# Optimization experiments

Hardware: AMD Instinct MI355X
Metric: run time of the kernel (lower is better)

Reference implementation:

```python
import jax, jax.numpy as jnp
import numpy as np

N = 20000
E = 320000
NEG_SLOPE = 0.2
BN_EPS = 1e-5


def _segment_softmax(e, dst, n):
    # e: [E, H] attention logits, dst: [E] destination node ids
    m = jax.ops.segment_max(e, dst, num_segments=n)           # [N, H]
    ex = jnp.exp(e - m[dst])                                   # [E, H]
    s = jax.ops.segment_sum(ex, dst, num_segments=n)          # [N, H]
    return ex / s[dst]


def gat_conv(x, src, dst, W, a_src, a_dst, b, heads, out_ch):
    # PyG GATConv (concat=True): h = x @ W reshaped to [N, H, C]
    n = x.shape[0]
    h = (x @ W).reshape(n, heads, out_ch)                      # [N, H, C]
    al_s = jnp.einsum('nhc,hc->nh', h, a_src)                  # [N, H]
    al_d = jnp.einsum('nhc,hc->nh', h, a_dst)
    e = jax.nn.leaky_relu(al_s[src] + al_d[dst], NEG_SLOPE)    # [E, H]
    alpha = _segment_softmax(e, dst, n)                        # [E, H]
    msg = h[src] * alpha[:, :, None]                           # [E, H, C]
    out = jax.ops.segment_sum(msg, dst, num_segments=n)        # [N, H, C]
    return out.reshape(n, heads * out_ch) + b


def batch_norm(x, gamma, beta):
    mu = jnp.mean(x, axis=0)
    var = jnp.mean((x - mu) ** 2, axis=0)  # biased, as torch BN training
    return gamma * (x - mu) * jax.lax.rsqrt(var + BN_EPS) + beta


def setup_inputs() -> dict:
    key = jax.random.key(0)
    ks = jax.random.split(key, 16)
    F_in, H1, C1 = 128, 8, 64
    D = H1 * C1  # 512
    OUT = 2
    def gl(k, shape, fan):
        return jax.random.normal(k, shape, dtype=jnp.float32) / np.sqrt(fan)
    x = jax.random.normal(ks[0], (N, F_in), dtype=jnp.float32)
    edge_index = jax.random.randint(ks[1], (2, E), 0, N, dtype=jnp.int64)
    return {
        'x': x, 'edge_index': edge_index,
        'W1': gl(ks[2], (F_in, H1 * C1), F_in),
        'a1s': gl(ks[3], (H1, C1), C1), 'a1d': gl(ks[4], (H1, C1), C1),
        'b1': jnp.zeros((D,), jnp.float32),
        'W2': gl(ks[5], (D, D), D),
        'a2s': gl(ks[6], (1, D), D), 'a2d': gl(ks[7], (1, D), D),
        'b2': jnp.zeros((D,), jnp.float32),
        'fc1_w': gl(ks[8], (D, D), D), 'fc1_b': jnp.zeros((D,), jnp.float32),
        'g1': jnp.ones((D,), jnp.float32), 'be1': jnp.zeros((D,), jnp.float32),
        'fc2_w': gl(ks[9], (D, D), D), 'fc2_b': jnp.zeros((D,), jnp.float32),
        'g2': jnp.ones((D,), jnp.float32), 'be2': jnp.zeros((D,), jnp.float32),
        'lin_w': gl(ks[10], (D, OUT), D), 'lin_b': jnp.zeros((OUT,), jnp.float32),
    }


def reference(x, edge_index, W1, a1s, a1d, b1, W2, a2s, a2d, b2,
              fc1_w, fc1_b, g1, be1, fc2_w, fc2_b, g2, be2, lin_w, lin_b):
    n = x.shape[0]
    loop = jnp.arange(n, dtype=edge_index.dtype)
    src = jnp.concatenate([edge_index[0], loop])  # add self-loops (PyG default)
    dst = jnp.concatenate([edge_index[1], loop])
    h = gat_conv(x, src, dst, W1, a1s, a1d, b1, heads=8, out_ch=64)
    h = batch_norm(jax.nn.relu(h @ fc1_w + fc1_b), g1, be1)
    h = gat_conv(h, src, dst, W2, a2s, a2d, b2, heads=1, out_ch=512)
    h = batch_norm(jax.nn.relu(h @ fc2_w + fc2_b), g2, be2)
    out = jax.nn.relu(h @ lin_w + lin_b)  # dropout p=0 is identity
    return out
```

## Files before the change

### kernel.cpp

```cpp
#include <hip/hip_runtime.h>
#include <hip/hip_bf16.h>

static constexpr int NN = 20000;
static constexpr int EE = 320000;
static constexpr int ET = EE + NN;
static constexpr int DD = 512;
static constexpr int FIN = 128;

typedef __attribute__((ext_vector_type(8))) short short8;
typedef __attribute__((ext_vector_type(4))) float f32x4;

__device__ __forceinline__ unsigned short f2bf(float f) {
    unsigned u = __float_as_uint(f);
    u += 0x7fffu + ((u >> 16) & 1u);
    return (unsigned short)(u >> 16);
}
__device__ __forceinline__ float bf2f(unsigned short b) {
    return __uint_as_float(((unsigned)b) << 16);
}

__device__ __forceinline__ void async_copy16(short* lds, const unsigned short* g) {
    __builtin_amdgcn_global_load_lds(
        (const __attribute__((address_space(1))) unsigned int*)g,
        (__attribute__((address_space(3))) unsigned int*)lds,
        16, 0, 0);
}

__global__ void scan_k(const int* __restrict__ deg, int* __restrict__ row_ptr,
                       int* __restrict__ perm) {
    __shared__ int part[1024];
    __shared__ int hist16[16][512];
    __shared__ int hbase[512];
    int t = threadIdx.x;
    int wv = t >> 6;
    for (int k = t; k < 16 * 512; k += 1024) ((int*)hist16)[k] = 0;
    __syncthreads();
    const int CH = (NN + 1023) / 1024;
    int start = t * CH;
    int end = min(start + CH, NN);
    int dl[CH];
    int s = 0;
    for (int i = start; i < end; ++i) {
        int d = deg[i] + 1;
        dl[i - start] = d;
        s += d;
        atomicAdd(&hist16[wv][min(d, 511)], 1);
    }
    part[t] = s;
    __syncthreads();
    if (t < 512) {
        int base = 0;
#pragma unroll
        for (int w = 0; w < 16; ++w) { int c = hist16[w][t]; hist16[w][t] = base; base += c; }
        hbase[t] = base;
    }
    for (int off = 1; off < 1024; off <<= 1) {
        int v = 0;
        if (t >= off) v = part[t - off];
        __syncthreads();
        part[t] += v;
        __syncthreads();
    }
    int base = (t == 0) ? 0 : part[t - 1];
    for (int i = start; i < end; ++i) { row_ptr[i] = base; base += dl[i - start]; }
    if (t == 1023) row_ptr[NN] = part[1023];
    if (t == 0) {
        int a = 0;
        for (int b2 = 0; b2 < 512; ++b2) { int c = hbase[b2]; hbase[b2] = a; a += c; }
    }
    __syncthreads();
    for (int i = start; i < end; ++i) {
        int d = min(dl[i - start], 511);
        int r = atomicAdd(&hist16[wv][d], 1);
        int pos = hbase[d] + r;
        perm[NN - 1 - pos] = i;
    }
}

static constexpr int TBLK = 208;
static constexpr int SZ_X4 = NN * FIN / 4;
static constexpr int XCB = (SZ_X4 + 255) / 256;
static constexpr int CDB = (EE + 255) / 256;
__global__ __launch_bounds__(256) void prep_all_k(
    const float* __restrict__ x, const float* __restrict__ W1,
    const float* __restrict__ fc1, const float* __restrict__ W2,
    const float* __restrict__ fc2,
    unsigned short* __restrict__ xb, unsigned short* __restrict__ W1t,
    unsigned short* __restrict__ fc1t, unsigned short* __restrict__ W2t,
    unsigned short* __restrict__ fc2t,
    const void* __restrict__ ei, int is64, int* __restrict__ deg) {
    int b = blockIdx.x;
    if (b < CDB) {
        int i = b * 256 + threadIdx.x;
        if (i < EE) {
            int d = is64 ? (int)((const long long*)ei)[EE + i] : ((const int*)ei)[EE + i];
            atomicAdd(&deg[d], 1);
        }
        return;
    }
    b -= CDB;
    if (b < TBLK) {
        __shared__ unsigned short tile[64][65];
        const float* src; unsigned short* dst; int rows, cols;
        if (b < 16)       { src = W1;  dst = W1t;  rows = FIN; cols = DD; }
        else if (b < 80)  { b -= 16;  src = fc1; dst = fc1t; rows = DD; cols = DD; }
        else if (b < 144) { b -= 80;  src = W2;  dst = W2t;  rows = DD; cols = DD; }
        else              { b -= 144; src = fc2; dst = fc2t; rows = DD; cols = DD; }
        int tc = cols / 64;
        int r0 = (b / tc) * 64, c0 = (b % tc) * 64;
        int t = threadIdx.x, lr = t >> 6, lc = t & 63;
#pragma unroll
        for (int p = 0; p < 16; ++p) {
            int r = lr + p * 4;
            tile[r][lc] = f2bf(src[(size_t)(r0 + r) * cols + c0 + lc]);
        }
        __syncthreads();
#pragma unroll
        for (int p = 0; p < 16; ++p) {
            int r = lr + p * 4;
            dst[(size_t)(c0 + r) * rows + r0 + lc] = tile[lc][r];
        }
        return;
    }
    int i = (b - TBLK) * 256 + threadIdx.x;
    if (i < SZ_X4) {
        float4 v = ((const float4*)x)[i];
        unsigned short o[4] = {f2bf(v.x), f2bf(v.y), f2bf(v.z), f2bf(v.w)};
        *(unsigned long long*)(xb + (size_t)i * 4) = *(const unsigned long long*)o;
    }
}

template <int RELU, int HASBIAS, int STATS, int ALS, int H, int FILLEX>
__global__ __launch_bounds__(256) void gemm_bf16(const unsigned short* __restrict__ A,
                                                 const unsigned short* __restrict__ Bt,
                                                 const float* __restrict__ bias,
                                                 unsigned short* __restrict__ Cb,
                                                 float* __restrict__ bnstat,
                                                 const float* __restrict__ avs,
                                                 const float* __restrict__ avd,
                                                 float* __restrict__ al_s,
                                                 float* __restrict__ al_d,
                                                 int M, int Nc, int K,
                                                 const void* __restrict__ ei, int is64,
                                                 const int* __restrict__ rp,
                                                 int* __restrict__ cursor,
                                                 int* __restrict__ csr_src,
                                                 int* __restrict__ csr_dst) {
    int id = blockIdx.x;
    if (FILLEX && id >= 640) {
        int e = (id - 640) * 256 + threadIdx.x;
        if (e >= ET) return;
        int s, d;
        if (e < EE) {
            if (is64) {
                const long long* p = (const long long*)ei;
                s = (int)p[e]; d = (int)p[EE + e];
            } else {
                const int* p = (const int*)ei;
                s = p[e]; d = p[EE + e];
            }
        } else {
            s = d = e - EE;
        }
        int pos = atomicAdd(&cursor[d], 1);
        int slot = rp[d] + pos;
        csr_src[slot] = s;
        csr_dst[slot] = d;
        return;
    }
    int bm = ((id >> 5) << 3) + (id & 7);
    int bn = (id >> 3) & 3;
    int m0 = bm * 128, n0 = bn * 128;
    if (m0 >= M) return;

    __shared__ short As0[128 * 32], As1[128 * 32];
    __shared__ short Bs0[128 * 32], Bs1[128 * 32];
    int t = threadIdx.x;
    int lane = t & 63, w = t >> 6;
    int wm = w & 1, wn = w >> 1;
    int quad = lane >> 4, mr = lane & 15;
    int lrow = lane >> 2;
    int lcol = (lane & 3) * 8;

    const unsigned short* Ag0 = A + (size_t)(m0 + w * 32 + lrow) * K + lcol;
    const unsigned short* Ag1 = A + (size_t)(m0 + w * 32 + 16 + lrow) * K + lcol;
    const unsigned short* Bg0 = Bt + (size_t)(n0 + w * 32 + lrow) * K + lcol;
    const unsigned short* Bg1 = Bt + (size_t)(n0 + w * 32 + 16 + lrow) * K + lcol;
    short* Al[2][2] = {{&As0[(w * 32) * 32], &As0[(w * 32 + 16) * 32]},
                       {&As1[(w * 32) * 32], &As1[(w * 32 + 16) * 32]}};
    short* Bl[2][2] = {{&Bs0[(w * 32) * 32], &Bs0[(w * 32 + 16) * 32]},
                       {&Bs1[(w * 32) * 32], &Bs1[(w * 32 + 16) * 32]}};

    f32x4 zero = {0.f, 0.f, 0.f, 0.f};
    f32x4 acc[4][4];
#pragma unroll
    for (int i = 0; i < 4; ++i)
#pragma unroll
        for (int j = 0; j < 4; ++j) acc[i][j] = zero;

    for (int k0 = 0; k0 < K; k0 += 64) {
        async_copy16(Al[0][0], Ag0 + k0);
        async_copy16(Al[1][0], Ag0 + k0 + 32);
        async_copy16(Al[0][1], Ag1 + k0);
        async_copy16(Al[1][1], Ag1 + k0 + 32);
        async_copy16(Bl[0][0], Bg0 + k0);
        async_copy16(Bl[1][0], Bg0 + k0 + 32);
        async_copy16(Bl[0][1], Bg1 + k0);
        async_copy16(Bl[1][1], Bg1 + k0 + 32);
        __syncthreads();
#pragma unroll
        for (int kp = 0; kp < 2; ++kp) {
            const short* Sa = kp ? As1 : As0;
            const short* Sb = kp ? Bs1 : Bs0;
            short8 af[4], bfr[4];
#pragma unroll
            for (int i = 0; i < 4; ++i) {
                af[i]  = *(const short8*)(&Sa[(wm * 64 + i * 16 + mr) * 32 + quad * 8]);
                bfr[i] = *(const short8*)(&Sb[(wn * 64 + i * 16 + mr) * 32 + quad * 8]);
            }
#pragma unroll
            for (int i = 0; i < 4; ++i)
#pragma unroll
                for (int j = 0; j < 4; ++j)
                    acc[i][j] = __builtin_amdgcn_mfma_f32_16x16x32_bf16(af[i], bfr[j], acc[i][j], 0, 0, 0);
        }
        __syncthreads();
    }

    float as_j[4], ad_j[4];
    if (ALS) {
#pragma unroll
        for (int j = 0; j < 4; ++j) {
            int n = n0 + wn * 64 + j * 16 + mr;
            as_j[j] = avs[n];
            ad_j[j] = avd[n];
        }
    }
    const int head = (H == 8) ? ((n0 + wn * 64) >> 6) : 0;
    float sj[4] = {0.f, 0.f, 0.f, 0.f}, qj[4] = {0.f, 0.f, 0.f, 0.f};
#pragma unroll
    for (int i = 0; i < 4; ++i) {
        int mb = m0 + wm * 64 + i * 16 + quad * 4;
#pragma unroll
        for (int r = 0; r < 4; ++r) {
            int m = mb + r;
            bool valid = (m < M);
            float ps = 0.f, pd = 0.f;
#pragma unroll
            for (int j = 0; j < 4; ++j) {
                int n = n0 + wn * 64 + j * 16 + mr;
                float v = acc[i][j][r];
                if (HASBIAS) v += bias[n];
                if (RELU) v = fmaxf(v, 0.f);
                unsigned short hb = f2bf(v);
                if (valid) Cb[(size_t)m * Nc + n] = hb;
                if (ALS) {
                    float vv = bf2f(hb);
                    ps += as_j[j] * vv;
                    pd += ad_j[j] * vv;
                }
                if (STATS && valid) { sj[j] += v; qj[j] += v * v; }
            }
            if (ALS) {
                ps += __shfl_xor(ps, 1); pd += __shfl_xor(pd, 1);
                ps += __shfl_xor(ps, 2); pd += __shfl_xor(pd, 2);
                ps += __shfl_xor(ps, 4); pd += __shfl_xor(pd, 4);
                ps += __shfl_xor(ps, 8); pd += __shfl_xor(pd, 8);
                if (mr == 0 && valid) {
                    if (H == 8) { al_s[m * 8 + head] = ps; al_d[m * 8 + head] = pd; }
                    else        { atomicAdd(&al_s[m], ps); atomicAdd(&al_d[m], pd); }
                }
            }
        }
    }
    if (STATS) {
#pragma unroll
        for (int j = 0; j < 4; ++j) {
            float s = sj[j], q = qj[j];
            s += __shfl_xor(s, 16); q += __shfl_xor(q, 16);
            s += __shfl_xor(s, 32); q += __shfl_xor(q, 32);
            if (lane < 16) {
                int n = n0 + wn * 64 + j * 16 + mr;
                atomicAdd(&bnstat[n], s);
                atomicAdd(&bnstat[512 + n], q);
            }
        }
    }
}

__global__ __launch_bounds__(256) void alpha1_k(const float* __restrict__ al_s,
                                                const float* __restrict__ al_d,
                                                const int* __restrict__ csr_src,
                                                const int* __restrict__ csr_dst,
                                                int2* __restrict__ ea) {
    int p = blockIdx.x * blockDim.x + threadIdx.x;
    if (p >= ET) return;
    int sn = csr_src[p], d = csr_dst[p];
    float4 s0 = *(const float4*)(al_s + (size_t)sn * 8);
    float4 s1 = *(const float4*)(al_s + (size_t)sn * 8 + 4);
    float4 d0 = *(const float4*)(al_d + (size_t)d * 8);
    float4 d1 = *(const float4*)(al_d + (size_t)d * 8 + 4);
    float l[8] = {s0.x + d0.x, s0.y + d0.y, s0.z + d0.z, s0.w + d0.w,
                  s1.x + d1.x, s1.y + d1.y, s1.z + d1.z, s1.w + d1.w};
#pragma unroll
    for (int h = 0; h < 8; ++h) {
        float xx = l[h];
        float a = __expf((xx > 0.f) ? xx : 0.2f * xx);
        ea[(size_t)h * ET + p] = make_int2(sn, __float_as_int(a));
    }
}

__global__ __launch_bounds__(256) void alpha2_k(const float* __restrict__ al_s,
                                                const float* __restrict__ al_d,
                                                const int* __restrict__ csr_src,
                                                const int* __restrict__ csr_dst,
                                                int2* __restrict__ ea) {
    int p = blockIdx.x * blockDim.x + threadIdx.x;
    if (p >= ET) return;
    int sn = csr_src[p], d = csr_dst[p];
    float xx = al_s[sn] + al_d[d];
    float a = __expf((xx > 0.f) ? xx : 0.2f * xx);
    ea[p] = make_int2(sn, __float_as_int(a));
}

template <int H>
__global__ __launch_bounds__(256) void gat_gather_k(const unsigned short* __restrict__ hb,
                                                    const int2* __restrict__ ea,
                                                    const int* __restrict__ row_ptr,
                                                    const int* __restrict__ perm,
                                                    const float* __restrict__ bias,
                                                    unsigned short* __restrict__ outb) {
    int b = blockIdx.x;
    int s = b & 7;
    int g = b >> 3;
    int t = threadIdx.x;
    int w = t >> 6, lane = t & 63;
    int grp = lane >> 3, cg = lane & 7;
    int n = perm[g * 32 + w * 8 + grp];
    int col = s * 64 + cg * 8;
    const int2* ep = ea + (H == 8 ? (size_t)s * ET : (size_t)0);
    const char* hbase = (const char*)hb + col * 2;
    int beg = row_ptr[n], end = row_ptr[n + 1];
    int last = end - 1;
    int nb = (end - beg + 7) >> 3;

    float acc[8] = {0.f, 0.f, 0.f, 0.f, 0.f, 0.f, 0.f, 0.f};
    float psum = 0.f;
    int2 v[8];
#pragma unroll
    for (int u = 0; u < 8; ++u) {
        int pp = beg + u;
        int2 r = ep[min(pp, last)];
        if (pp > last) r.y = 0;
        v[u] = r;
    }
    for (int bb = 1; bb <= nb; ++bb) {
        short8 hreg[8];
#pragma unroll
        for (int u = 0; u < 8; ++u)
            hreg[u] = *(const short8*)(hbase + ((unsigned)v[u].x << 10));
        float av[8];
#pragma unroll
        for (int u = 0; u < 8; ++u) av[u] = __int_as_float(v[u].y);
        int2 vn[8];
        if (bb < nb) {
            int p0 = beg + bb * 8;
#pragma unroll
            for (int u = 0; u < 8; ++u) {
                int pp = p0 + u;
                int2 r = ep[min(pp, last)];
                if (pp > last) r.y = 0;
                vn[u] = r;
            }
        }
#pragma unroll
        for (int u = 0; u < 8; ++u) psum += av[u];
#pragma unroll
        for (int u = 0; u < 8; ++u)
#pragma unroll
            for (int j = 0; j < 8; ++j)
                acc[j] = fmaf(av[u], bf2f((unsigned short)hreg[u][j]), acc[j]);
        if (bb < nb) {
#pragma unroll
            for (int u = 0; u < 8; ++u) v[u] = vn[u];
        }
    }
    float inv = 1.0f / psum;
    unsigned short ov[8];
#pragma unroll
    for (int j = 0; j < 8; ++j) ov[j] = f2bf(acc[j] * inv + bias[col + j]);
    *(int4*)(outb + (size_t)n * DD + col) = *(const int4*)ov;
}

__global__ __launch_bounds__(256) void fold1_k(const float* __restrict__ stat,
                                               const float* __restrict__ g,
                                               const float* __restrict__ be,
                                               unsigned short* __restrict__ W2t,
                                               float* __restrict__ bias2) {
    int t = threadIdx.x;
    int n = blockIdx.x * 4 + (t >> 6);
    int lane = t & 63;
    float pb = 0.f;
#pragma unroll
    for (int j = 0; j < 8; ++j) {
        int k = lane * 8 + j;
        float mean = stat[k] * (1.0f / NN);
        float var = stat[512 + k] * (1.0f / NN) - mean * mean;
        float sc = g[k] * rsqrtf(var + 1e-5f);
        float sh = be[k] - mean * sc;
        float wv = bf2f(W2t[n * DD + k]);
        W2t[n * DD + k] = f2bf(sc * wv);
        pb += sh * wv;
    }
    for (int off = 32; off; off >>= 1) pb += __shfl_down(pb, off);
    if (lane == 0) bias2[n] = pb;
}

__global__ void final_linear(const unsigned short* __restrict__ xb,
                             const float* __restrict__ stat, const float* __restrict__ g,
                             const float* __restrict__ be, const float* __restrict__ w,
                             const float* __restrict__ b, float* __restrict__ out) {
    int wave = (blockIdx.x * blockDim.x + threadIdx.x) >> 6;
    int lane = threadIdx.x & 63;
    if (wave >= NN) return;
    short8 hv = *(const short8*)(xb + (size_t)wave * DD + lane * 8);
    float p0 = 0.f, p1 = 0.f;
#pragma unroll
    for (int j = 0; j < 8; ++j) {
        int c = lane * 8 + j;
        float mean = stat[c] * (1.0f / NN);
        float var = stat[512 + c] * (1.0f / NN) - mean * mean;
        float sc = g[c] * rsqrtf(var + 1e-5f);
        float vn = (bf2f((unsigned short)hv[j]) - mean) * sc + be[c];
        p0 += vn * w[2 * c];
        p1 += vn * w[2 * c + 1];
    }
    for (int off = 32; off; off >>= 1) {
        p0 += __shfl_down(p0, off);
        p1 += __shfl_down(p1, off);
    }
    if (lane == 0) {
        out[wave * 2 + 0] = fmaxf(p0 + b[0], 0.f);
        out[wave * 2 + 1] = fmaxf(p1 + b[1], 0.f);
    }
}

extern "C" void kernel_launch(void* const* d_in, const int* in_sizes, int n_in,
                              void* d_out, int out_size, void* d_ws, size_t ws_size,
                              hipStream_t stream) {
    const float* x     = (const float*)d_in[0];
    const void*  ei    = d_in[1];
    const float* W1    = (const float*)d_in[2];
    const float* a1s   = (const float*)d_in[3];
    const float* a1d   = (const float*)d_in[4];
    const float* b1    = (const float*)d_in[5];
    const float* W2    = (const float*)d_in[6];
    const float* a2s   = (const float*)d_in[7];
    const float* a2d   = (const float*)d_in[8];
    const float* b2    = (const float*)d_in[9];
    const float* fc1_w = (const float*)d_in[10];
    const float* fc1_b = (const float*)d_in[11];
    const float* g1    = (const float*)d_in[12];
    const float* be1   = (const float*)d_in[13];
    const float* fc2_w = (const float*)d_in[14];
    const float* fc2_b = (const float*)d_in[15];
    const float* g2    = (const float*)d_in[16];
    const float* be2   = (const float*)d_in[17];
    const float* lin_w = (const float*)d_in[18];
    const float* lin_b = (const float*)d_in[19];
    float* out = (float*)d_out;

    char* ws = (char*)d_ws;
    auto alloc = [&](size_t bytes) {
        void* p = (void*)ws;
        ws += (bytes + 255) & ~size_t(255);
        return p;
    };
    unsigned short* h_bf    = (unsigned short*)alloc((size_t)NN * DD * 2);
    unsigned short* act_bf  = (unsigned short*)alloc((size_t)NN * DD * 2);
    unsigned short* W1t     = (unsigned short*)alloc((size_t)DD * FIN * 2);
    unsigned short* fc1t    = (unsigned short*)alloc((size_t)DD * DD * 2);
    unsigned short* W2t     = (unsigned short*)alloc((size_t)DD * DD * 2);
    unsigned short* fc2t    = (unsigned short*)alloc((size_t)DD * DD * 2);
    float*          al_s    = (float*)alloc((size_t)NN * 8 * 4);
    float*          al_d    = (float*)alloc((size_t)NN * 8 * 4);
    int*            row_ptr = (int*)alloc((size_t)(NN + 1) * 4);
    int*            csr_src = (int*)alloc((size_t)ET * 4);
    int*            csr_dst = (int*)alloc((size_t)ET * 4);
    int*            perm    = (int*)alloc((size_t)NN * 4);
    float*          bias2f  = (float*)alloc(512 * 4);
    int2*           ea      = (int2*)alloc((size_t)8 * ET * 8);
    int*            deg     = (int*)alloc((size_t)2 * NN * 4);
    int*            cursor  = deg + NN;
    float*          bnstatA = (float*)alloc((size_t)(2048 + 2 * NN) * 4);
    float*          bnstatB = bnstatA + 1024;
    float*          al_s2   = bnstatA + 2048;
    float*          al_d2   = al_s2 + NN;

    const int is64 = (in_sizes[1] >= (int)(2u * EE * 8u)) ? 1 : 0;

    hipMemsetAsync(deg, 0, (size_t)2 * NN * 4, stream);
    hipMemsetAsync(bnstatA, 0, (size_t)(2048 + 2 * NN) * 4, stream);

    unsigned short* x_bf = act_bf;
    const int prep_blocks = CDB + TBLK + XCB;
    prep_all_k<<<prep_blocks, 256, 0, stream>>>(x, W1, fc1_w, W2, fc2_w,
                                                x_bf, W1t, fc1t, W2t, fc2t,
                                                ei, is64, deg);
    scan_k<<<1, 1024, 0, stream>>>(deg, row_ptr, perm);

    const int GB = 640;
    const int FB = (ET + 255) / 256;
    const int GGB = 8 * (NN / 32);
    const int AB = (ET + 255) / 256;

    gemm_bf16<0, 0, 0, 1, 8, 1><<<GB + FB, 256, 0, stream>>>(
        x_bf, W1t, nullptr, h_bf, nullptr, a1s, a1d, al_s, al_d, NN, DD, FIN,
        ei, is64, row_ptr, cursor, csr_src, csr_dst);
    alpha1_k<<<AB, 256, 0, stream>>>(al_s, al_d, csr_src, csr_dst, ea);
    gat_gather_k<8><<<GGB, 256, 0, stream>>>(h_bf, ea, row_ptr, perm, b1, act_bf);
    gemm_bf16<1, 1, 1, 0, 8, 0><<<GB, 256, 0, stream>>>(
        act_bf, fc1t, fc1_b, h_bf, bnstatA, nullptr, nullptr, nullptr, nullptr, NN, DD, DD,
        nullptr, 0, nullptr, nullptr, nullptr, nullptr);
    fold1_k<<<128, 256, 0, stream>>>(bnstatA, g1, be1, W2t, bias2f);

    gemm_bf16<0, 1, 0, 1, 1, 0><<<GB, 256, 0, stream>>>(
        h_bf, W2t, bias2f, act_bf, nullptr, a2s, a2d, al_s2, al_d2, NN, DD, DD,
        nullptr, 0, nullptr, nullptr, nullptr, nullptr);
    alpha2_k<<<AB, 256, 0, stream>>>(al_s2, al_d2, csr_src, csr_dst, ea);
    gat_gather_k<1><<<GGB, 256, 0, stream>>>(act_bf, ea, row_ptr, perm, b2, h_bf);
    gemm_bf16<1, 1, 1, 0, 8, 0><<<GB, 256, 0, stream>>>(
        h_bf, fc2t, fc2_b, act_bf, bnstatB, nullptr, nullptr, nullptr, nullptr, NN, DD, DD,
        nullptr, 0, nullptr, nullptr, nullptr, nullptr);

    final_linear<<<(NN + 3) / 4, 256, 0, stream>>>(act_bf, bnstatB, g2, be2, lin_w, lin_b, out);
}
```

Baseline: 343.7 us.

## Pad CSR rows to multiples of eight and fold final batchnorm into linear

After: 336.6 us. 1.02x faster.

```diff
diff --git a/kernel.cpp b/kernel.cpp
--- a/kernel.cpp
+++ b/kernel.cpp
@@ -6,6 +6,7 @@
 static constexpr int ET = EE + NN;
 static constexpr int DD = 512;
 static constexpr int FIN = 128;
+static constexpr int ETP_MAX = ET + 7 * NN;
 
 typedef __attribute__((ext_vector_type(8))) short short8;
 typedef __attribute__((ext_vector_type(4))) float f32x4;
@@ -31,6 +32,7 @@
     __shared__ int part[1024];
     __shared__ int hist16[16][512];
     __shared__ int hbase[512];
+    __shared__ int btot[512];
     int t = threadIdx.x;
     int wv = t >> 6;
     for (int k = t; k < 16 * 512; k += 1024) ((int*)hist16)[k] = 0;
@@ -43,7 +45,7 @@
     for (int i = start; i < end; ++i) {
         int d = deg[i] + 1;
         dl[i - start] = d;
-        s += d;
+        s += (d + 7) & ~7;
         atomicAdd(&hist16[wv][min(d, 511)], 1);
     }
     part[t] = s;
@@ -52,8 +54,18 @@
         int base = 0;
 #pragma unroll
         for (int w = 0; w < 16; ++w) { int c = hist16[w][t]; hist16[w][t] = base; base += c; }
+        btot[t] = base;
         hbase[t] = base;
     }
+    __syncthreads();
+    for (int off = 1; off < 512; off <<= 1) {
+        int v = 0;
+        if (t < 512 && t >= off) v = hbase[t - off];
+        __syncthreads();
+        if (t < 512) hbase[t] += v;
+        __syncthreads();
+    }
+    if (t < 512) hbase[t] -= btot[t];
     for (int off = 1; off < 1024; off <<= 1) {
         int v = 0;
         if (t >= off) v = part[t - off];
@@ -62,13 +74,8 @@
         __syncthreads();
     }
     int base = (t == 0) ? 0 : part[t - 1];
-    for (int i = start; i < end; ++i) { row_ptr[i] = base; base += dl[i - start]; }
+    for (int i = start; i < end; ++i) { row_ptr[i] = base; base += (dl[i - start] + 7) & ~7; }
     if (t == 1023) row_ptr[NN] = part[1023];
-    if (t == 0) {
-        int a = 0;
-        for (int b2 = 0; b2 < 512; ++b2) { int c = hbase[b2]; hbase[b2] = a; a += c; }
-    }
-    __syncthreads();
     for (int i = start; i < end; ++i) {
         int d = min(dl[i - start], 511);
         int r = atomicAdd(&hist16[wv][d], 1);
@@ -292,10 +299,18 @@
                                                 const float* __restrict__ al_d,
                                                 const int* __restrict__ csr_src,
                                                 const int* __restrict__ csr_dst,
+                                                const int* __restrict__ row_ptr,
                                                 int2* __restrict__ ea) {
     int p = blockIdx.x * blockDim.x + threadIdx.x;
-    if (p >= ET) return;
-    int sn = csr_src[p], d = csr_dst[p];
+    if (p >= row_ptr[NN]) return;
+    int sn = csr_src[p];
+    if (sn < 0) {
+        int2 z = make_int2(0, 0);
+#pragma unroll
+        for (int h = 0; h < 8; ++h) ea[(size_t)h * ETP_MAX + p] = z;
+        return;
+    }
+    int d = csr_dst[p];
     float4 s0 = *(const float4*)(al_s + (size_t)sn * 8);
     float4 s1 = *(const float4*)(al_s + (size_t)sn * 8 + 4);
     float4 d0 = *(const float4*)(al_d + (size_t)d * 8);
@@ -306,7 +321,7 @@
     for (int h = 0; h < 8; ++h) {
         float xx = l[h];
         float a = __expf((xx > 0.f) ? xx : 0.2f * xx);
-        ea[(size_t)h * ET + p] = make_int2(sn, __float_as_int(a));
+        ea[(size_t)h * ETP_MAX + p] = make_int2(sn, __float_as_int(a));
     }
 }
 
@@ -314,10 +329,13 @@
                                                 const float* __restrict__ al_d,
                                                 const int* __restrict__ csr_src,
                                                 const int* __restrict__ csr_dst,
+                                                const int* __restrict__ row_ptr,
                                                 int2* __restrict__ ea) {
     int p = blockIdx.x * blockDim.x + threadIdx.x;
-    if (p >= ET) return;
-    int sn = csr_src[p], d = csr_dst[p];
+    if (p >= row_ptr[NN]) return;
+    int sn = csr_src[p];
+    if (sn < 0) { ea[p] = make_int2(0, 0); return; }
+    int d = csr_dst[p];
     float xx = al_s[sn] + al_d[d];
     float a = __expf((xx > 0.f) ? xx : 0.2f * xx);
     ea[p] = make_int2(sn, __float_as_int(a));
@@ -338,22 +356,16 @@
     int grp = lane >> 3, cg = lane & 7;
     int n = perm[g * 32 + w * 8 + grp];
     int col = s * 64 + cg * 8;
-    const int2* ep = ea + (H == 8 ? (size_t)s * ET : (size_t)0);
+    const int2* ep = ea + (H == 8 ? (size_t)s * ETP_MAX : (size_t)0);
     const char* hbase = (const char*)hb + col * 2;
-    int beg = row_ptr[n], end = row_ptr[n + 1];
-    int last = end - 1;
-    int nb = (end - beg + 7) >> 3;
+    int beg = row_ptr[n];
+    int nb = (row_ptr[n + 1] - beg) >> 3;
 
     float acc[8] = {0.f, 0.f, 0.f, 0.f, 0.f, 0.f, 0.f, 0.f};
     float psum = 0.f;
     int2 v[8];
 #pragma unroll
-    for (int u = 0; u < 8; ++u) {
-        int pp = beg + u;
-        int2 r = ep[min(pp, last)];
-        if (pp > last) r.y = 0;
-        v[u] = r;
-    }
+    for (int u = 0; u < 8; ++u) v[u] = ep[beg + u];
     for (int bb = 1; bb <= nb; ++bb) {
         short8 hreg[8];
 #pragma unroll
@@ -366,12 +378,7 @@
         if (bb < nb) {
             int p0 = beg + bb * 8;
 #pragma unroll
-            for (int u = 0; u < 8; ++u) {
-                int pp = p0 + u;
-                int2 r = ep[min(pp, last)];
-                if (pp > last) r.y = 0;
-                vn[u] = r;
-            }
+            for (int u = 0; u < 8; ++u) vn[u] = ep[p0 + u];
         }
 #pragma unroll
         for (int u = 0; u < 8; ++u) psum += av[u];
@@ -416,10 +423,32 @@
     if (lane == 0) bias2[n] = pb;
 }
 
+__global__ void bnfold2_k(const float* __restrict__ stat, const float* __restrict__ g,
+                          const float* __restrict__ be, const float* __restrict__ lw,
+                          const float* __restrict__ lb, float* __restrict__ w01,
+                          float* __restrict__ kk) {
+    __shared__ float r0[512], r1[512];
+    int c = threadIdx.x;
+    float mean = stat[c] * (1.0f / NN);
+    float var = stat[512 + c] * (1.0f / NN) - mean * mean;
+    float sc = g[c] * rsqrtf(var + 1e-5f);
+    float sh = be[c] - mean * sc;
+    float w0 = lw[2 * c], w1 = lw[2 * c + 1];
+    w01[2 * c] = sc * w0;
+    w01[2 * c + 1] = sc * w1;
+    r0[c] = sh * w0;
+    r1[c] = sh * w1;
+    __syncthreads();
+    for (int off = 256; off; off >>= 1) {
+        if (c < off) { r0[c] += r0[c + off]; r1[c] += r1[c + off]; }
+        __syncthreads();
+    }
+    if (c == 0) { kk[0] = r0[0] + lb[0]; kk[1] = r1[0] + lb[1]; }
+}
+
 __global__ void final_linear(const unsigned short* __restrict__ xb,
-                             const float* __restrict__ stat, const float* __restrict__ g,
-                             const float* __restrict__ be, const float* __restrict__ w,
-                             const float* __restrict__ b, float* __restrict__ out) {
+                             const float* __restrict__ w01, const float* __restrict__ kk,
+                             float* __restrict__ out) {
     int wave = (blockIdx.x * blockDim.x + threadIdx.x) >> 6;
     int lane = threadIdx.x & 63;
     if (wave >= NN) return;
@@ -428,20 +457,17 @@
 #pragma unroll
     for (int j = 0; j < 8; ++j) {
         int c = lane * 8 + j;
-        float mean = stat[c] * (1.0f / NN);
-        float var = stat[512 + c] * (1.0f / NN) - mean * mean;
-        float sc = g[c] * rsqrtf(var + 1e-5f);
-        float vn = (bf2f((unsigned short)hv[j]) - mean) * sc + be[c];
-        p0 += vn * w[2 * c];
-        p1 += vn * w[2 * c + 1];
+        float h = bf2f((unsigned short)hv[j]);
+        p0 = fmaf(h, w01[2 * c], p0);
+        p1 = fmaf(h, w01[2 * c + 1], p1);
     }
     for (int off = 32; off; off >>= 1) {
         p0 += __shfl_down(p0, off);
         p1 += __shfl_down(p1, off);
     }
     if (lane == 0) {
-        out[wave * 2 + 0] = fmaxf(p0 + b[0], 0.f);
-        out[wave * 2 + 1] = fmaxf(p1 + b[1], 0.f);
+        out[wave * 2 + 0] = fmaxf(p0 + kk[0], 0.f);
+        out[wave * 2 + 1] = fmaxf(p1 + kk[1], 0.f);
     }
 }
 
@@ -485,22 +511,25 @@
     float*          al_s    = (float*)alloc((size_t)NN * 8 * 4);
     float*          al_d    = (float*)alloc((size_t)NN * 8 * 4);
     int*            row_ptr = (int*)alloc((size_t)(NN + 1) * 4);
-    int*            csr_src = (int*)alloc((size_t)ET * 4);
-    int*            csr_dst = (int*)alloc((size_t)ET * 4);
+    int*            csr_dst = (int*)alloc((size_t)ETP_MAX * 4);
     int*            perm    = (int*)alloc((size_t)NN * 4);
     float*          bias2f  = (float*)alloc(512 * 4);
-    int2*           ea      = (int2*)alloc((size_t)8 * ET * 8);
+    float*          w01     = (float*)alloc(1024 * 4);
+    float*          kkc     = (float*)alloc(256);
+    int2*           ea      = (int2*)alloc((size_t)8 * ETP_MAX * 8);
     int*            deg     = (int*)alloc((size_t)2 * NN * 4);
     int*            cursor  = deg + NN;
     float*          bnstatA = (float*)alloc((size_t)(2048 + 2 * NN) * 4);
     float*          bnstatB = bnstatA + 1024;
     float*          al_s2   = bnstatA + 2048;
     float*          al_d2   = al_s2 + NN;
+    int*            csr_src = (int*)alloc((size_t)ETP_MAX * 4);
 
     const int is64 = (in_sizes[1] >= (int)(2u * EE * 8u)) ? 1 : 0;
 
     hipMemsetAsync(deg, 0, (size_t)2 * NN * 4, stream);
     hipMemsetAsync(bnstatA, 0, (size_t)(2048 + 2 * NN) * 4, stream);
+    hipMemsetAsync(csr_src, 0xFF, (size_t)ETP_MAX * 4, stream);
 
     unsigned short* x_bf = act_bf;
     const int prep_blocks = CDB + TBLK + XCB;
@@ -512,12 +541,12 @@
     const int GB = 640;
     const int FB = (ET + 255) / 256;
     const int GGB = 8 * (NN / 32);
-    const int AB = (ET + 255) / 256;
+    const int AB = (ETP_MAX + 255) / 256;
 
     gemm_bf16<0, 0, 0, 1, 8, 1><<<GB + FB, 256, 0, stream>>>(
         x_bf, W1t, nullptr, h_bf, nullptr, a1s, a1d, al_s, al_d, NN, DD, FIN,
         ei, is64, row_ptr, cursor, csr_src, csr_dst);
-    alpha1_k<<<AB, 256, 0, stream>>>(al_s, al_d, csr_src, csr_dst, ea);
+    alpha1_k<<<AB, 256, 0, stream>>>(al_s, al_d, csr_src, csr_dst, row_ptr, ea);
     gat_gather_k<8><<<GGB, 256, 0, stream>>>(h_bf, ea, row_ptr, perm, b1, act_bf);
     gemm_bf16<1, 1, 1, 0, 8, 0><<<GB, 256, 0, stream>>>(
         act_bf, fc1t, fc1_b, h_bf, bnstatA, nullptr, nullptr, nullptr, nullptr, NN, DD, DD,
@@ -527,11 +556,12 @@
     gemm_bf16<0, 1, 0, 1, 1, 0><<<GB, 256, 0, stream>>>(
         h_bf, W2t, bias2f, act_bf, nullptr, a2s, a2d, al_s2, al_d2, NN, DD, DD,
         nullptr, 0, nullptr, nullptr, nullptr, nullptr);
-    alpha2_k<<<AB, 256, 0, stream>>>(al_s2, al_d2, csr_src, csr_dst, ea);
+    alpha2_k<<<AB, 256, 0, stream>>>(al_s2, al_d2, csr_src, csr_dst, row_ptr, ea);
     gat_gather_k<1><<<GGB, 256, 0, stream>>>(act_bf, ea, row_ptr, perm, b2, h_bf);
     gemm_bf16<1, 1, 1, 0, 8, 0><<<GB, 256, 0, stream>>>(
         h_bf, fc2t, fc2_b, act_bf, bnstatB, nullptr, nullptr, nullptr, nullptr, NN, DD, DD,
         nullptr, 0, nullptr, nullptr, nullptr, nullptr);
 
-    final_linear<<<(NN + 3) / 4, 256, 0, stream>>>(act_bf, bnstatB, g2, be2, lin_w, lin_b, out);
-}
+    bnfold2_k<<<1, 512, 0, stream>>>(bnstatB, g2, be2, lin_w, lin_b, w01, kkc);
+    final_linear<<<(NN + 3) / 4, 256, 0, stream>>>(act_bf, w01, kkc, out);
+}
```
